# Kernel optimization log

Measured on AMD Instinct MI355X. Metric: run time of the kernel, lower is better.

Reference implementation:

```python
import jax, jax.numpy as jnp
import numpy as np

LAYER_NUM = 2
NUM_CLS = 128
HIDDEN = 256
NUM_NODES = 1024


def setup_inputs() -> dict:
    key = jax.random.key(0)
    ks = jax.random.split(key, 12)
    s = 0.05
    return {
        "x": jax.random.normal(ks[0], (NUM_NODES, HIDDEN), jnp.float32),
        "knowledge": jax.random.uniform(ks[1], (NUM_CLS, NUM_CLS), jnp.float32) / NUM_CLS,
        "w3w": jax.random.normal(ks[2], (HIDDEN, 2 * HIDDEN), jnp.float32) * s,
        "b3w": jax.random.normal(ks[3], (HIDDEN,), jnp.float32) * s,
        "u3": jax.random.normal(ks[4], (HIDDEN, HIDDEN), jnp.float32) * s,
        "bu3": jax.random.normal(ks[5], (HIDDEN,), jnp.float32) * s,
        "w4w": jax.random.normal(ks[6], (HIDDEN, 2 * HIDDEN), jnp.float32) * s,
        "b4w": jax.random.normal(ks[7], (HIDDEN,), jnp.float32) * s,
        "w5w": jax.random.normal(ks[8], (HIDDEN, 2 * HIDDEN), jnp.float32) * s,
        "b5w": jax.random.normal(ks[9], (HIDDEN,), jnp.float32) * s,
        "u5": jax.random.normal(ks[10], (HIDDEN, HIDDEN), jnp.float32) * s,
        "bu5": jax.random.normal(ks[11], (HIDDEN,), jnp.float32) * s,
    }


def reference(x, knowledge, w3w, b3w, u3, bu3, w4w, b4w, w5w, b5w, u5, bu5):
    N, H = x.shape
    C = knowledge.shape[0]
    # hidden[n, c, :] = x[n, :]  (repeat per class)
    hidden = jnp.broadcast_to(x[:, None, :], (N, C, H))
    for _ in range(LAYER_NUM):
        hs = hidden.sum(0)                      # [C, H]
        diff = hs[None, :, :] - hidden          # [N, C, H]
        # knowledge.T @ diff_n  and  knowledge @ diff_n, vectorized over nodes
        left = jnp.einsum('kc,nkh->nch', knowledge, diff)
        right = jnp.einsum('ck,nkh->nch', knowledge, diff)
        av = jnp.concatenate([left, right], axis=-1).reshape(N * C, 2 * H)
        h = hidden.reshape(N * C, H)
        uh3 = h @ u3.T + bu3                    # shared: rv uses fc_eq3_u (source quirk)
        zv = jax.nn.sigmoid(av @ w3w.T + b3w + uh3)
        rv = jax.nn.sigmoid(av @ w4w.T + b4w + uh3)
        hv = jnp.tanh(av @ w5w.T + b5w + (rv * h) @ u5.T + bu5)
        h = (1.0 - zv) * h + zv * hv
        hidden = h.reshape(N, C, H)
    return hidden
```

## Files before the change

kernel.cpp:

```cpp
#include <hip/hip_runtime.h>
#include <cstdint>
#include <cstddef>


#define NODES 1024
#define NCLS  128
#define HID   256

using frag  = __attribute__((ext_vector_type(8))) short;
using frag4 = __attribute__((ext_vector_type(4))) short;
using f32x4 = __attribute__((ext_vector_type(4))) float;

__device__ __forceinline__ float bf2f(unsigned short h){
  unsigned int u = ((unsigned int)h) << 16;
  float f; __builtin_memcpy(&f, &u, 4); return f;
}
__device__ __forceinline__ unsigned short f2bf(float f){
  unsigned int u; __builtin_memcpy(&u, &f, 4);
  u = (u + 0x7fffu + ((u >> 16) & 1u)) >> 16;
  return (unsigned short)u;
}
__device__ __forceinline__ float sigm(float x){ return 1.0f/(1.0f + __expf(-x)); }
__device__ __forceinline__ float tanh_fast(float x){ return 1.0f - 2.0f/(__expf(2.0f*x) + 1.0f); }

#define GLOBAL_AS(p) ((const __attribute__((address_space(1))) void*)(p))
#define LDS_AS(p)    ((__attribute__((address_space(3))) void*)(p))

template<int OUT_BF16>
__global__ __launch_bounds__(256) void gemm_bf16(
    const unsigned short* __restrict__ A0, int ldA0, int K0,
    const unsigned short* __restrict__ A1, int ldA1,
    const unsigned short* __restrict__ BT, int ldB, long bStride,
    void* __restrict__ Cptr, int ldC,
    int Ntiles, int Ktot, unsigned int aMask, int Mtiles)
{
  __shared__ unsigned short As[4096];
  __shared__ unsigned short Bs[4096];
  const int t   = threadIdx.x;
  const int bid = blockIdx.x;
  const int xcd = bid & 7, slot = bid >> 3;
  const int mtPerX = (Mtiles >= 8) ? (Mtiles >> 3) : 1;
  const int mt = xcd * mtPerX + slot / Ntiles;
  const int nt = slot % Ntiles;
  const int lane = t & 63, w = t >> 6;
  const int wm = w >> 1, wn = w & 1;
  const int r = lane & 15, q = lane >> 4;
  const int m0 = mt * 128, n0 = nt * 128;
  const unsigned short* Bbase = BT + (size_t)mt * (size_t)bStride;

  f32x4 acc[4][4] = {};

  for (int kb = 0; kb < Ktot; kb += 32) {
#pragma unroll
    for (int i = 0; i < 2; ++i) {
      int u  = i * 256 + t;
      int mi = u >> 2;
      int kc = (u & 3) * 8;
      int k  = kb + kc;
      const unsigned short* ga;
      if (k < K0) ga = A0 + (size_t)((unsigned int)(m0 + mi) & aMask) * (size_t)ldA0 + k;
      else        ga = A1 + (size_t)(m0 + mi) * (size_t)ldA1 + (k - K0);
      __builtin_amdgcn_global_load_lds(GLOBAL_AS(ga), LDS_AS(&As[u * 8]), 16, 0, 0);
      const unsigned short* gb = Bbase + (size_t)(n0 + mi) * (size_t)ldB + k;
      __builtin_amdgcn_global_load_lds(GLOBAL_AS(gb), LDS_AS(&Bs[u * 8]), 16, 0, 0);
    }
    __syncthreads();

    frag af[4], bf_[4];
#pragma unroll
    for (int x = 0; x < 4; ++x) {
      af[x]  = *(const frag*)&As[(wm * 64 + x * 16 + r) * 32 + q * 8];
      bf_[x] = *(const frag*)&Bs[(wn * 64 + x * 16 + r) * 32 + q * 8];
    }
#pragma unroll
    for (int x = 0; x < 4; ++x)
#pragma unroll
      for (int y = 0; y < 4; ++y)
        acc[x][y] = __builtin_amdgcn_mfma_f32_16x16x32_bf16(af[x], bf_[y], acc[x][y], 0, 0, 0);
    __syncthreads();
  }

#pragma unroll
  for (int x = 0; x < 4; ++x) {
#pragma unroll
    for (int y = 0; y < 4; ++y) {
      int col = n0 + wn * 64 + y * 16 + r;
#pragma unroll
      for (int g = 0; g < 4; ++g) {
        long row = m0 + wm * 64 + x * 16 + q * 4 + g;
        if (OUT_BF16) ((unsigned short*)Cptr)[row * (long)ldC + col] = f2bf(acc[x][y][g]);
        else          ((float*)Cptr)[row * (long)ldC + col] = acc[x][y][g];
      }
    }
  }
}

__global__ __launch_bounds__(256, 4) void gemm_pre(
    const unsigned short* __restrict__ AVH, const unsigned short* __restrict__ H1,
    const unsigned short* __restrict__ WB, unsigned short* __restrict__ PRE)
{
  __shared__ unsigned short As[8192];
  __shared__ unsigned short Bs[8192];
  const int t   = threadIdx.x;
  const int bid = blockIdx.x;
  const int xcd = bid & 7, slot = bid >> 3;
  const int mt = xcd * 128 + slot / 6;
  const int ct = slot % 6;
  const int lane = t & 63, w = t >> 6;
  const int wm = w >> 1, wn = w & 1;
  const int r = lane & 15, q = lane >> 4;
  const int m0 = mt * 128;
  const unsigned short* Wrow = WB + (size_t)(ct * 128) * 768;

  f32x4 acc[4][4] = {};

  for (int kb = 0; kb < 512; kb += 64) {
#pragma unroll
    for (int i = 0; i < 4; ++i) {
      int u  = i * 256 + t;
      int mi = u >> 3;
      int gc = (u & 7) ^ (mi & 7);
      __builtin_amdgcn_global_load_lds(GLOBAL_AS(AVH + (size_t)(m0 + mi) * 512 + kb + gc * 8),
                                       LDS_AS(&As[u * 8]), 16, 0, 0);
      __builtin_amdgcn_global_load_lds(GLOBAL_AS(Wrow + (size_t)mi * 768 + kb + gc * 8),
                                       LDS_AS(&Bs[u * 8]), 16, 0, 0);
    }
    __syncthreads();
#pragma unroll
    for (int kh = 0; kh < 2; ++kh) {
      frag af[4], bf_[4];
#pragma unroll
      for (int x = 0; x < 4; ++x) {
        int ra = wm * 64 + x * 16 + r;
        int rb = wn * 64 + x * 16 + r;
        af[x]  = *(const frag*)&As[ra * 64 + (((kh * 4 + q) ^ (ra & 7)) * 8)];
        bf_[x] = *(const frag*)&Bs[rb * 64 + (((kh * 4 + q) ^ (rb & 7)) * 8)];
      }
#pragma unroll
      for (int x = 0; x < 4; ++x)
#pragma unroll
        for (int y = 0; y < 4; ++y)
          acc[x][y] = __builtin_amdgcn_mfma_f32_16x16x32_bf16(af[x], bf_[y], acc[x][y], 0, 0, 0);
    }
    __syncthreads();
  }

  if (ct < 4) {
    for (int kb = 0; kb < 256; kb += 64) {
#pragma unroll
      for (int i = 0; i < 4; ++i) {
        int u  = i * 256 + t;
        int mi = u >> 3;
        int gc = (u & 7) ^ (mi & 7);
        __builtin_amdgcn_global_load_lds(GLOBAL_AS(H1 + (size_t)(m0 + mi) * 256 + kb + gc * 8),
                                         LDS_AS(&As[u * 8]), 16, 0, 0);
        __builtin_amdgcn_global_load_lds(GLOBAL_AS(Wrow + (size_t)mi * 768 + 512 + kb + gc * 8),
                                         LDS_AS(&Bs[u * 8]), 16, 0, 0);
      }
      __syncthreads();
#pragma unroll
      for (int kh = 0; kh < 2; ++kh) {
        frag af[4], bf_[4];
#pragma unroll
        for (int x = 0; x < 4; ++x) {
          int ra = wm * 64 + x * 16 + r;
          int rb = wn * 64 + x * 16 + r;
          af[x]  = *(const frag*)&As[ra * 64 + (((kh * 4 + q) ^ (ra & 7)) * 8)];
          bf_[x] = *(const frag*)&Bs[rb * 64 + (((kh * 4 + q) ^ (rb & 7)) * 8)];
        }
#pragma unroll
        for (int x = 0; x < 4; ++x)
#pragma unroll
          for (int y = 0; y < 4; ++y)
            acc[x][y] = __builtin_amdgcn_mfma_f32_16x16x32_bf16(af[x], bf_[y], acc[x][y], 0, 0, 0);
      }
      __syncthreads();
    }
  }

#pragma unroll
  for (int x = 0; x < 4; ++x) {
#pragma unroll
    for (int y = 0; y < 4; ++y) {
      int col = ct * 128 + wn * 64 + y * 16 + r;
#pragma unroll
      for (int g = 0; g < 4; ++g) {
        long row = m0 + wm * 64 + x * 16 + q * 4 + g;
        PRE[row * 768 + col] = f2bf(acc[x][y][g]);
      }
    }
  }
}

__global__ __launch_bounds__(256) void gemm_l1(
    const float* __restrict__ XW, const float* __restrict__ SW,
    const float* __restrict__ x,
    const float* __restrict__ b3, const float* __restrict__ b4,
    const float* __restrict__ b5, const float* __restrict__ bu3,
    const float* __restrict__ bu5,
    const float* __restrict__ colsum, const float* __restrict__ rowsum,
    const unsigned short* __restrict__ u5b,
    const unsigned short* __restrict__ KTbN, const unsigned short* __restrict__ KbN,
    unsigned short* __restrict__ H1, unsigned short* __restrict__ AVH)
{
  __shared__ unsigned short SM[17408];
  unsigned short* As = SM;
  unsigned short* Bs = SM + 4096;
  unsigned short* L  = SM;
  __shared__ float tP1[256], tP2[256], tP3[256], tX[256];
  __shared__ float tZ1[256], tZ2[256], tZ3[256];
  __shared__ float tV1[256], tV2[256], tV3[256];
  __shared__ float tCS[128], tRS[128];

  const int t = threadIdx.x, bid = blockIdx.x;
  const int xcd = bid & 7, slot = bid >> 3;
  const int n  = xcd * 128 + (slot >> 1);
  const int nt = slot & 1;
  const int lane = t & 63, w = t >> 6, wm = w >> 1, wn = w & 1;
  const int r = lane & 15, q = lane >> 4;
  const int n0 = nt * 128;
  const float* xw = XW + (size_t)n * 1792;

  {
    int i = t;
    float xwi0 = xw[i], xwi1 = xw[256 + i], xwi2 = xw[512 + i], xwi3 = xw[768 + i];
    float xwi4 = xw[1024 + i], xwi5 = xw[1280 + i], xwu = xw[1536 + i];
    tP1[i] = SW[512 + i] - xwi2;
    tP2[i] = SW[768 + i] - xwi3;
    tP3[i] = xwu + b4[i] + bu3[i];
    tX[i]  = x[(size_t)n * HID + i];
    tZ1[i] = SW[i] - xwi0;
    tZ2[i] = SW[256 + i] - xwi1;
    tZ3[i] = xwu + b3[i] + bu3[i];
    tV1[i] = SW[1024 + i] - xwi4;
    tV2[i] = SW[1280 + i] - xwi5;
    tV3[i] = b5[i] + bu5[i];
    if (t < 128) { tCS[t] = colsum[t]; tRS[t] = rowsum[t]; }
  }
  __syncthreads();

  f32x4 acc[4][4] = {};

  for (int kb = 0; kb < 256; kb += 32) {
#pragma unroll
    for (int i = 0; i < 2; ++i) {
      int u  = i * 256 + t;
      int mi = u >> 2;
      int c  = u & 3;
      int kc = c * 8;
      int k  = kb + kc;
      int gc = c ^ (mi & 3);
      __builtin_amdgcn_global_load_lds(GLOBAL_AS(u5b + (size_t)(n0 + mi) * 256 + kb + gc * 8),
                                       LDS_AS(&Bs[u * 8]), 16, 0, 0);
      float cs = tCS[mi], rs = tRS[mi];
      frag a;
#pragma unroll
      for (int e = 0; e < 8; ++e) {
        int i2 = k + e;
        float pre = cs * tP1[i2] + rs * tP2[i2] + tP3[i2];
        a[e] = (short)f2bf(sigm(pre) * tX[i2]);
      }
      *(frag*)&As[mi * 32 + (c ^ (mi & 3)) * 8] = a;
    }
    __syncthreads();

    frag af[4], bf_[4];
#pragma unroll
    for (int xx = 0; xx < 4; ++xx) {
      int ra = wm * 64 + xx * 16 + r;
      int rb = wn * 64 + xx * 16 + r;
      af[xx]  = *(const frag*)&As[ra * 32 + ((q ^ (ra & 3)) * 8)];
      bf_[xx] = *(const frag*)&Bs[rb * 32 + ((q ^ (rb & 3)) * 8)];
    }
#pragma unroll
    for (int xx = 0; xx < 4; ++xx)
#pragma unroll
      for (int y = 0; y < 4; ++y)
        acc[xx][y] = __builtin_amdgcn_mfma_f32_16x16x32_bf16(af[xx], bf_[y], acc[xx][y], 0, 0, 0);
    __syncthreads();
  }

#pragma unroll
  for (int xx = 0; xx < 4; ++xx) {
#pragma unroll
    for (int y = 0; y < 4; ++y) {
      int j = wn * 64 + y * 16 + r;
      int i = n0 + j;
      frag4 pack;
#pragma unroll
      for (int g = 0; g < 4; ++g) {
        int c = wm * 64 + xx * 16 + q * 4 + g;
        float cs = tCS[c], rs = tRS[c];
        float z  = sigm(cs * tZ1[i] + rs * tZ2[i] + tZ3[i]);
        float p5 = cs * tV1[i] + rs * tV2[i] + tV3[i] + acc[xx][y][g];
        float h1 = (1.0f - z) * tX[i] + z * tanh_fast(p5);
        unsigned short hb = f2bf(h1);
        pack[g] = (short)hb;
        H1[(size_t)(n * 128 + c) * HID + i] = hb;
      }
      *(frag4*)&L[j * 136 + (wm * 64 + xx * 16 + q * 4)] = pack;
    }
  }
  __syncthreads();

#pragma unroll
  for (int s = 0; s < 2; ++s) {
    const unsigned short* Ks = s ? KbN : KTbN;
    f32x4 a2[4][4] = {};
#pragma unroll
    for (int kb = 0; kb < 4; ++kb) {
      frag af[4], bf_[4];
#pragma unroll
      for (int xx = 0; xx < 4; ++xx) {
        int cp = wm * 64 + xx * 16 + r;
        af[xx] = *(const frag*)(Ks + (size_t)cp * 128 + kb * 32 + q * 8);
        int j = wn * 64 + xx * 16 + r;
        bf_[xx] = *(const frag*)&L[j * 136 + kb * 32 + q * 8];
      }
#pragma unroll
      for (int xx = 0; xx < 4; ++xx)
#pragma unroll
        for (int y = 0; y < 4; ++y)
          a2[xx][y] = __builtin_amdgcn_mfma_f32_16x16x32_bf16(af[xx], bf_[y], a2[xx][y], 0, 0, 0);
    }
#pragma unroll
    for (int xx = 0; xx < 4; ++xx)
#pragma unroll
      for (int y = 0; y < 4; ++y) {
        int col = s * 256 + n0 + wn * 64 + y * 16 + r;
#pragma unroll
        for (int g = 0; g < 4; ++g) {
          int cp = wm * 64 + xx * 16 + q * 4 + g;
          AVH[(size_t)(n * 128 + cp) * 512 + col] = f2bf(a2[xx][y][g]);
        }
      }
  }
}

__global__ __launch_bounds__(256) void gemm_l2(
    const unsigned short* __restrict__ PRE, const float* __restrict__ SG,
    const unsigned short* __restrict__ H1, const unsigned short* __restrict__ u5b,
    float* __restrict__ out)
{
  __shared__ unsigned short As[4096], Bs[4096];
  const int t = threadIdx.x, bid = blockIdx.x;
  const int xcd = bid & 7, slot = bid >> 3;
  const int mt = xcd * 128 + (slot >> 1);
  const int nt = slot & 1;
  const int lane = t & 63, w = t >> 6, wm = w >> 1, wn = w & 1;
  const int r = lane & 15, q = lane >> 4;
  const int m0 = mt * 128, n0 = nt * 128;

  f32x4 acc[4][4] = {};

  for (int kb = 0; kb < 256; kb += 32) {
#pragma unroll
    for (int i = 0; i < 2; ++i) {
      int u  = i * 256 + t;
      int mi = u >> 2;
      int c  = u & 3;
      int k  = kb + c * 8;
      int gc = c ^ (mi & 3);
      __builtin_amdgcn_global_load_lds(GLOBAL_AS(u5b + (size_t)(n0 + mi) * 256 + kb + gc * 8),
                                       LDS_AS(&Bs[u * 8]), 16, 0, 0);
      long row = m0 + mi;
      frag p4 = *(const frag*)(PRE + row * 768 + 256 + k);
      frag h1 = *(const frag*)(H1 + row * 256 + k);
      const float* sg = SG + (size_t)mi * 768 + 256 + k;
      frag a;
#pragma unroll
      for (int e = 0; e < 8; ++e) {
        float rv = sigm(sg[e] + bf2f((unsigned short)p4[e]));
        a[e] = (short)f2bf(rv * bf2f((unsigned short)h1[e]));
      }
      *(frag*)&As[mi * 32 + (c ^ (mi & 3)) * 8] = a;
    }
    __syncthreads();

    frag af[4], bf_[4];
#pragma unroll
    for (int xx = 0; xx < 4; ++xx) {
      int ra = wm * 64 + xx * 16 + r;
      int rb = wn * 64 + xx * 16 + r;
      af[xx]  = *(const frag*)&As[ra * 32 + ((q ^ (ra & 3)) * 8)];
      bf_[xx] = *(const frag*)&Bs[rb * 32 + ((q ^ (rb & 3)) * 8)];
    }
#pragma unroll
    for (int xx = 0; xx < 4; ++xx)
#pragma unroll
      for (int y = 0; y < 4; ++y)
        acc[xx][y] = __builtin_amdgcn_mfma_f32_16x16x32_bf16(af[xx], bf_[y], acc[xx][y], 0, 0, 0);
    __syncthreads();
  }

#pragma unroll
  for (int xx = 0; xx < 4; ++xx) {
#pragma unroll
    for (int y = 0; y < 4; ++y) {
      int i = n0 + wn * 64 + y * 16 + r;
#pragma unroll
      for (int g = 0; g < 4; ++g) {
        int c = wm * 64 + xx * 16 + q * 4 + g;
        long row = m0 + c;
        float z  = sigm(SG[(size_t)c * 768 + i] + bf2f(PRE[row * 768 + i]));
        float pv = SG[(size_t)c * 768 + 512 + i] + bf2f(PRE[row * 768 + 512 + i])
                 + acc[xx][y][g];
        float h  = bf2f(H1[row * 256 + i]);
        out[row * 256 + i] = (1.0f - z) * h + z * tanh_fast(pv);
      }
    }
  }
}

__global__ __launch_bounds__(256) void prep_cast(
    const float* __restrict__ x, const float* __restrict__ Kn,
    const float* __restrict__ w3, const float* __restrict__ u3,
    const float* __restrict__ w4, const float* __restrict__ w5,
    const float* __restrict__ u5,
    unsigned short* __restrict__ xb, unsigned short* __restrict__ WB,
    unsigned short* __restrict__ WB2, unsigned short* __restrict__ u5b,
    unsigned short* __restrict__ KbN, unsigned short* __restrict__ KTbN)
{
  int idx = blockIdx.x * 256 + threadIdx.x;
  if (idx < 262144) { xb[idx] = f2bf(x[idx]); return; }
  idx -= 262144;
  if (idx < 589824) {
    int col = idx / 768, j = idx % 768;
    int g = col >> 8, i = col & 255;
    float v;
    if (j < 512) { const float* wg = (g == 0) ? w3 : (g == 1) ? w4 : w5; v = wg[(size_t)i * 512 + j]; }
    else v = (g < 2) ? u3[(size_t)i * 256 + (j - 512)] : 0.0f;
    WB[(size_t)col * 768 + j] = f2bf(v);
    return;
  }
  idx -= 589824;
  if (idx < 458752) {
    int col = idx / 256, h = idx % 256;
    int b = col >> 8, i = col & 255;
    float v = (b < 6) ? ((b < 2 ? w3 : (b < 4 ? w4 : w5))[(size_t)i * 512 + (b & 1) * 256 + h])
                      : u3[(size_t)i * 256 + h];
    WB2[(size_t)col * 256 + h] = f2bf(v);
    return;
  }
  idx -= 458752;
  if (idx < 65536) { u5b[idx] = f2bf(u5[idx]); return; }
  idx -= 65536;
  if (idx < 16384) { int c = idx >> 7, k = idx & 127; KbN[idx]  = f2bf(-Kn[c * 128 + k]); return; }
  idx -= 16384;
  { int c = idx >> 7, k = idx & 127; KTbN[idx] = f2bf(-Kn[k * 128 + c]); }
}

__global__ __launch_bounds__(256) void prep_reduce(
    const float* __restrict__ x, const float* __restrict__ Kn,
    float* __restrict__ S, float* __restrict__ colsum, float* __restrict__ rowsum)
{
  int b = blockIdx.x, t = threadIdx.x;
  if (b < 8) {
    float s = 0.f;
    for (int n = 0; n < 128; ++n) s += x[(size_t)(b * 128 + n) * HID + t];
    atomicAdd(&S[t], s);
  } else if (b == 8) {
    if (t < NCLS) { float s = 0.f; for (int k = 0; k < NCLS; ++k) s += Kn[k * NCLS + t]; colsum[t] = s; }
  } else {
    if (t < NCLS) { float s = 0.f; for (int k = 0; k < NCLS; ++k) s += Kn[t * NCLS + k]; rowsum[t] = s; }
  }
}

__global__ __launch_bounds__(256) void prep_sw(
    const float* __restrict__ S, const float* __restrict__ w3,
    const float* __restrict__ w4, const float* __restrict__ w5, float* __restrict__ SW)
{
  int col = blockIdx.x * 256 + threadIdx.x;
  int b = col >> 8, i = col & 255;
  const float* w = (b < 2) ? w3 : (b < 4) ? w4 : w5;
  const float* row = w + (size_t)i * 512 + (b & 1) * 256;
  float s = 0.f;
  for (int h = 0; h < HID; ++h) s += S[h] * row[h];
  SW[col] = s;
}

__global__ __launch_bounds__(256) void reduce_hs(
    const unsigned short* __restrict__ H1, float* __restrict__ hs)
{
  int bid = blockIdx.x;
  int c = bid >> 5, nch = bid & 31;
  int i = threadIdx.x;
  const unsigned short* p = H1 + (size_t)nch * 32 * NCLS * HID + (size_t)c * HID + i;
  float s = 0.f;
  for (int n = 0; n < 32; ++n) s += bf2f(p[(size_t)n * NCLS * HID]);
  atomicAdd(&hs[c * HID + i], s);
}

__global__ __launch_bounds__(256) void p2a(
    const float* __restrict__ hs, const float* __restrict__ w3,
    const float* __restrict__ w4, const float* __restrict__ w5, float* __restrict__ hsW)
{
  __shared__ float hrow[HID];
  int k = blockIdx.x & 127, b = blockIdx.x >> 7;
  int t = threadIdx.x;
  hrow[t] = hs[k * HID + t];
  __syncthreads();
  const float* w = (b < 2) ? w3 : (b < 4) ? w4 : w5;
  const float* row = w + (size_t)t * 512 + (b & 1) * 256;
  float s = 0.f;
  for (int h = 0; h < HID; ++h) s += hrow[h] * row[h];
  hsW[(size_t)k * 1536 + b * 256 + t] = s;
}

__global__ __launch_bounds__(256) void p2b(
    const float* __restrict__ hsW, const float* __restrict__ Kn,
    const float* __restrict__ b3, const float* __restrict__ b4, const float* __restrict__ b5,
    const float* __restrict__ bu3, const float* __restrict__ bu5, float* __restrict__ SG)
{
  __shared__ float kc[NCLS], kr[NCLS];
  int c = blockIdx.x, t = threadIdx.x;
  if (t < NCLS) { kc[t] = Kn[t * NCLS + c]; kr[t] = Kn[c * NCLS + t]; }
  __syncthreads();
  for (int g = 0; g < 3; ++g) {
    int i = t;
    const float* L = hsW + (size_t)(2 * g) * 256 + i;
    const float* R = hsW + (size_t)(2 * g + 1) * 256 + i;
    float s = 0.f;
    for (int k = 0; k < NCLS; ++k) s += kc[k] * L[(size_t)k * 1536] + kr[k] * R[(size_t)k * 1536];
    const float* bg = (g == 0) ? b3 : (g == 1) ? b4 : b5;
    s += bg[i] + ((g < 2) ? bu3[i] : bu5[i]);
    SG[(size_t)c * 768 + g * 256 + i] = s;
  }
}

extern "C" void kernel_launch(void* const* d_in, const int* in_sizes, int n_in,
                              void* d_out, int out_size, void* d_ws, size_t ws_size,
                              hipStream_t stream) {
  (void)in_sizes; (void)n_in; (void)out_size; (void)ws_size;
  const float* x   = (const float*)d_in[0];
  const float* Kn  = (const float*)d_in[1];
  const float* w3  = (const float*)d_in[2];
  const float* b3  = (const float*)d_in[3];
  const float* u3  = (const float*)d_in[4];
  const float* bu3 = (const float*)d_in[5];
  const float* w4  = (const float*)d_in[6];
  const float* b4  = (const float*)d_in[7];
  const float* w5  = (const float*)d_in[8];
  const float* b5  = (const float*)d_in[9];
  const float* u5  = (const float*)d_in[10];
  const float* bu5 = (const float*)d_in[11];
  float* out = (float*)d_out;

  char* w = (char*)d_ws;
  unsigned short* AVH = (unsigned short*)(w);
  unsigned short* PRE = (unsigned short*)(w + 134217728);
  unsigned short* H1  = (unsigned short*)(w + 335544320);
  float*          XW  = (float*)(w + 402653184);
  char* misc = w + 409993216;
  float* S      = (float*)(misc);
  float* hs     = (float*)(misc + 1024);
  float* SW     = (float*)(misc + 132096);
  float* colsum = (float*)(misc + 138240);
  float* rowsum = (float*)(misc + 138752);
  float* hsW    = (float*)(misc + 139264);
  float* SG     = (float*)(misc + 925696);
  unsigned short* WB   = (unsigned short*)(misc + 1318912);
  unsigned short* WB2  = (unsigned short*)(misc + 2498560);
  unsigned short* u5b  = (unsigned short*)(misc + 3416064);
  unsigned short* KbN  = (unsigned short*)(misc + 3547136);
  unsigned short* KTbN = (unsigned short*)(misc + 3579904);
  unsigned short* xb   = (unsigned short*)(misc + 3612672);

  hipMemsetAsync(misc, 0, 132096, stream);

  prep_cast<<<5504, 256, 0, stream>>>(x, Kn, w3, u3, w4, w5, u5, xb, WB, WB2, u5b, KbN, KTbN);
  prep_reduce<<<10, 256, 0, stream>>>(x, Kn, S, colsum, rowsum);
  prep_sw<<<6, 256, 0, stream>>>(S, w3, w4, w5, SW);

  gemm_bf16<0><<<8 * 14, 256, 0, stream>>>(xb, 256, 256, xb, 256, WB2, 256, 0L,
                                           (void*)XW, 1792, 14, 256, 0xFFFFFFFFu, 8);
  gemm_l1<<<2048, 256, 0, stream>>>(XW, SW, x, b3, b4, b5, bu3, bu5,
                                    colsum, rowsum, u5b, KTbN, KbN, H1, AVH);

  reduce_hs<<<4096, 256, 0, stream>>>(H1, hs);
  p2a<<<768, 256, 0, stream>>>(hs, w3, w4, w5, hsW);
  p2b<<<128, 256, 0, stream>>>(hsW, Kn, b3, b4, b5, bu3, bu5, SG);

  gemm_pre<<<6144, 256, 0, stream>>>(AVH, H1, WB, PRE);

  gemm_l2<<<2048, 256, 0, stream>>>(PRE, SG, H1, u5b, out);
}
```

Baseline: 776.7 us.

## Double-buffer gemm_pre K loop and stage output through LDS for coalesced stores

Rewrites the gemm_pre main loop as a single double-buffered pipeline with K-step 32, so global-to-LDS loads for the next stage are issued while MFMAs run on the current one. It also merges the AVH and H1 phases into one loop. The epilogue now writes accumulators to a swizzled LDS tile and then stores 16-byte vectors to PRE, replacing scattered 2-byte stores. The smaller K step doubles the number of barriers per tile, and the epilogue adds an extra LDS round trip.

Result: faster. 709.9 us (-8.6%).

```diff
diff --git a/kernel.cpp b/kernel.cpp
--- a/kernel.cpp
+++ b/kernel.cpp
@@ -99,8 +99,7 @@
     const unsigned short* __restrict__ AVH, const unsigned short* __restrict__ H1,
     const unsigned short* __restrict__ WB, unsigned short* __restrict__ PRE)
 {
-  __shared__ unsigned short As[8192];
-  __shared__ unsigned short Bs[8192];
+  __shared__ __align__(16) unsigned short SM[16384];
   const int t   = threadIdx.x;
   const int bid = blockIdx.x;
   const int xcd = bid & 7, slot = bid >> 3;
@@ -111,84 +110,71 @@
   const int r = lane & 15, q = lane >> 4;
   const int m0 = mt * 128;
   const unsigned short* Wrow = WB + (size_t)(ct * 128) * 768;
+  const int nst = (ct < 4) ? 24 : 16;
 
   f32x4 acc[4][4] = {};
 
-  for (int kb = 0; kb < 512; kb += 64) {
-#pragma unroll
-    for (int i = 0; i < 4; ++i) {
+  auto STAGE = [&](int b, int kt) {
+    const int kb = kt * 32;
+    unsigned short* Asb = SM + b * 4096;
+    unsigned short* Bsb = SM + 8192 + b * 4096;
+#pragma unroll
+    for (int i = 0; i < 2; ++i) {
       int u  = i * 256 + t;
-      int mi = u >> 3;
-      int gc = (u & 7) ^ (mi & 7);
-      __builtin_amdgcn_global_load_lds(GLOBAL_AS(AVH + (size_t)(m0 + mi) * 512 + kb + gc * 8),
-                                       LDS_AS(&As[u * 8]), 16, 0, 0);
+      int mi = u >> 2;
+      int gc = (u & 3) ^ (mi & 3);
+      const unsigned short* ga;
+      if (kb < 512) ga = AVH + (size_t)(m0 + mi) * 512 + kb + gc * 8;
+      else          ga = H1  + (size_t)(m0 + mi) * 256 + (kb - 512) + gc * 8;
+      __builtin_amdgcn_global_load_lds(GLOBAL_AS(ga), LDS_AS(&Asb[u * 8]), 16, 0, 0);
       __builtin_amdgcn_global_load_lds(GLOBAL_AS(Wrow + (size_t)mi * 768 + kb + gc * 8),
-                                       LDS_AS(&Bs[u * 8]), 16, 0, 0);
-    }
-    __syncthreads();
-#pragma unroll
-    for (int kh = 0; kh < 2; ++kh) {
-      frag af[4], bf_[4];
-#pragma unroll
-      for (int x = 0; x < 4; ++x) {
-        int ra = wm * 64 + x * 16 + r;
-        int rb = wn * 64 + x * 16 + r;
-        af[x]  = *(const frag*)&As[ra * 64 + (((kh * 4 + q) ^ (ra & 7)) * 8)];
-        bf_[x] = *(const frag*)&Bs[rb * 64 + (((kh * 4 + q) ^ (rb & 7)) * 8)];
-      }
-#pragma unroll
-      for (int x = 0; x < 4; ++x)
-#pragma unroll
-        for (int y = 0; y < 4; ++y)
-          acc[x][y] = __builtin_amdgcn_mfma_f32_16x16x32_bf16(af[x], bf_[y], acc[x][y], 0, 0, 0);
-    }
-    __syncthreads();
-  }
-
-  if (ct < 4) {
-    for (int kb = 0; kb < 256; kb += 64) {
-#pragma unroll
-      for (int i = 0; i < 4; ++i) {
-        int u  = i * 256 + t;
-        int mi = u >> 3;
-        int gc = (u & 7) ^ (mi & 7);
-        __builtin_amdgcn_global_load_lds(GLOBAL_AS(H1 + (size_t)(m0 + mi) * 256 + kb + gc * 8),
-                                         LDS_AS(&As[u * 8]), 16, 0, 0);
-        __builtin_amdgcn_global_load_lds(GLOBAL_AS(Wrow + (size_t)mi * 768 + 512 + kb + gc * 8),
-                                         LDS_AS(&Bs[u * 8]), 16, 0, 0);
-      }
-      __syncthreads();
-#pragma unroll
-      for (int kh = 0; kh < 2; ++kh) {
-        frag af[4], bf_[4];
-#pragma unroll
-        for (int x = 0; x < 4; ++x) {
-          int ra = wm * 64 + x * 16 + r;
-          int rb = wn * 64 + x * 16 + r;
-          af[x]  = *(const frag*)&As[ra * 64 + (((kh * 4 + q) ^ (ra & 7)) * 8)];
-          bf_[x] = *(const frag*)&Bs[rb * 64 + (((kh * 4 + q) ^ (rb & 7)) * 8)];
-        }
-#pragma unroll
-        for (int x = 0; x < 4; ++x)
-#pragma unroll
-          for (int y = 0; y < 4; ++y)
-            acc[x][y] = __builtin_amdgcn_mfma_f32_16x16x32_bf16(af[x], bf_[y], acc[x][y], 0, 0, 0);
-      }
-      __syncthreads();
-    }
-  }
-
-#pragma unroll
-  for (int x = 0; x < 4; ++x) {
+                                       LDS_AS(&Bsb[u * 8]), 16, 0, 0);
+    }
+  };
+
+  STAGE(0, 0);
+  __syncthreads();
+  int cur = 0;
+  for (int kt = 0; kt < nst; ++kt) {
+    if (kt + 1 < nst) STAGE(cur ^ 1, kt + 1);
+    const unsigned short* Asb = SM + cur * 4096;
+    const unsigned short* Bsb = SM + 8192 + cur * 4096;
+    frag af[4], bf_[4];
+#pragma unroll
+    for (int x = 0; x < 4; ++x) {
+      int ra = wm * 64 + x * 16 + r;
+      int rb = wn * 64 + x * 16 + r;
+      af[x]  = *(const frag*)&Asb[ra * 32 + ((q ^ (ra & 3)) * 8)];
+      bf_[x] = *(const frag*)&Bsb[rb * 32 + ((q ^ (rb & 3)) * 8)];
+    }
+#pragma unroll
+    for (int x = 0; x < 4; ++x)
+#pragma unroll
+      for (int y = 0; y < 4; ++y)
+        acc[x][y] = __builtin_amdgcn_mfma_f32_16x16x32_bf16(af[x], bf_[y], acc[x][y], 0, 0, 0);
+    __syncthreads();
+    cur ^= 1;
+  }
+
+  unsigned short* L = SM;
+#pragma unroll
+  for (int x = 0; x < 4; ++x)
 #pragma unroll
     for (int y = 0; y < 4; ++y) {
-      int col = ct * 128 + wn * 64 + y * 16 + r;
+      int j = wn * 64 + y * 16 + r;
 #pragma unroll
       for (int g = 0; g < 4; ++g) {
-        long row = m0 + wm * 64 + x * 16 + q * 4 + g;
-        PRE[row * 768 + col] = f2bf(acc[x][y][g]);
-      }
-    }
+        int c = wm * 64 + x * 16 + q * 4 + g;
+        L[c * 128 + (((j >> 3) ^ (c & 7)) * 8) + (j & 7)] = f2bf(acc[x][y][g]);
+      }
+    }
+  __syncthreads();
+#pragma unroll
+  for (int it = 0; it < 8; ++it) {
+    int unit = it * 256 + t;
+    int row = unit >> 4, gr = unit & 15;
+    frag v = *(const frag*)&L[row * 128 + ((gr ^ (row & 7)) * 8)];
+    *(frag*)&PRE[(size_t)(m0 + row) * 768 + ct * 128 + gr * 8] = v;
   }
 }
 
```
